# Kernel tuning notes

Measured on AMD Instinct MI355X. Metric: run time of the kernel, lower is better.

The kernel has to match this reference:

```python
import jax, jax.numpy as jnp
import numpy as np

S = 24; N = S * S; D = 1024; B = 4; H = 8; HD = D // H; K = 8
LN_EPS = 1e-5


def _spiral_indices(s, clockwise):
    inds = []
    top, bottom, left, right = 0, s - 1, 0, s - 1
    if clockwise:
        while top <= bottom and left <= right:
            for j in range(left, right + 1):
                inds.append((top, j))
            top += 1
            for i in range(top, bottom + 1):
                inds.append((i, right))
            right -= 1
            if top <= bottom:
                for j in range(right, left - 1, -1):
                    inds.append((bottom, j))
                bottom -= 1
            if left <= right:
                for i in range(bottom, top - 1, -1):
                    inds.append((i, left))
                left += 1
    else:
        while top <= bottom and left <= right:
            for i in range(top, bottom + 1):
                inds.append((i, left))
            left += 1
            for j in range(left, right + 1):
                inds.append((bottom, j))
            bottom -= 1
            if left <= right:
                for i in range(bottom, top - 1, -1):
                    inds.append((i, right))
                right -= 1
            if top <= bottom:
                for j in range(right, left - 1, -1):
                    inds.append((top, j))
                top += 1
    return np.array([i * s + j for i, j in inds], dtype=np.int32)


def _diag_indices(s, anti):
    idx = []
    for offset in (range(2 * s - 1) if anti else range(-(s - 1), s)):
        for i in range(s):
            j = (offset - i) if anti else (i + offset)
            if 0 <= j < s:
                idx.append(i * s + j)
    return np.array(idx, dtype=np.int32)


def _build_scan_indices(s):
    # Composite (scan + restore) permutation per direction: out_i = Linear_i(x[:, idx_i])
    ar = np.arange(s * s, dtype=np.int32).reshape(s, s)
    lr = ar.reshape(-1)                      # left_right: identity
    rl_scan = ar[:, ::-1].reshape(-1)        # right_left scan
    rl_restore = ar[:, ::-1].reshape(-1)     # restore flips width back
    rl = rl_scan[rl_restore]                 # composes to identity
    tb = ar.T.reshape(-1)                    # top_bottom (restore is plain view -> no inverse!)
    bt_scan = ar[::-1, :].T.reshape(-1)      # bottom_top scan: flip(transpose) flatten
    bt_restore = ar[::-1, :].reshape(-1)     # restore: view->transpose->flip(2)->transpose
    bt = bt_scan[bt_restore]
    dm = _diag_indices(s, anti=False)        # restore is plain view
    da = _diag_indices(s, anti=True)
    sc = _spiral_indices(s, clockwise=True)
    scc = _spiral_indices(s, clockwise=False)
    return np.stack([lr, rl, tb, bt, dm, da, sc, scc], axis=0)  # [8, N]


def setup_inputs() -> dict:
    key = jax.random.key(0)
    ks = jax.random.split(key, 12)
    sc = D ** -0.5
    return {
        "vision_features": jax.random.normal(ks[0], (B, N, D), dtype=jnp.float32),
        "dir_W": jax.random.normal(ks[1], (K, D, D), dtype=jnp.float32) * sc,
        "dir_b": jax.random.normal(ks[2], (K, D), dtype=jnp.float32) * 0.01,
        "in_proj_w": jax.random.normal(ks[3], (3 * D, D), dtype=jnp.float32) * sc,
        "in_proj_b": jax.random.normal(ks[4], (3 * D,), dtype=jnp.float32) * 0.01,
        "out_proj_w": jax.random.normal(ks[5], (D, D), dtype=jnp.float32) * sc,
        "out_proj_b": jax.random.normal(ks[6], (D,), dtype=jnp.float32) * 0.01,
        "fin_w": jax.random.normal(ks[7], (D, D), dtype=jnp.float32) * sc,
        "fin_b": jax.random.normal(ks[8], (D,), dtype=jnp.float32) * 0.01,
        "ln_g": jnp.ones((D,), dtype=jnp.float32),
        "ln_b": jnp.zeros((D,), dtype=jnp.float32),
        "scan_idx": jnp.asarray(_build_scan_indices(S)),  # [8, N] int32
    }


def reference(vision_features, dir_W, dir_b, in_proj_w, in_proj_b,
              out_proj_w, out_proj_b, fin_w, fin_b, ln_g, ln_b, scan_idx):
    b, n, d = vision_features.shape
    # Fused per-direction gather + batched GEMM: [B,8,N,D]
    gathered = vision_features[:, scan_idx]                     # [B,K,N,D]
    dirs = jnp.einsum('bknd,kde->bkne', gathered, dir_W) + dir_b[None, :, None, :]
    kv = dirs.reshape(b, K * n, d)                              # [B,8N,D]
    # MultiheadAttention (batch_first, 8 heads, eval -> no dropout)
    wq, wk, wv = in_proj_w[:d], in_proj_w[d:2 * d], in_proj_w[2 * d:]
    bq, bk, bv = in_proj_b[:d], in_proj_b[d:2 * d], in_proj_b[2 * d:]
    q = (vision_features @ wq.T + bq).reshape(b, n, H, HD).transpose(0, 2, 1, 3)
    k = (kv @ wk.T + bk).reshape(b, K * n, H, HD).transpose(0, 2, 1, 3)
    v = (kv @ wv.T + bv).reshape(b, K * n, H, HD).transpose(0, 2, 1, 3)
    scores = jnp.einsum('bhnd,bhmd->bhnm', q, k) / jnp.sqrt(jnp.asarray(HD, q.dtype))
    attn = jax.nn.softmax(scores, axis=-1)
    o = jnp.einsum('bhnm,bhmd->bhnd', attn, v).transpose(0, 2, 1, 3).reshape(b, n, d)
    fused = o @ out_proj_w.T + out_proj_b
    # output_projection: Linear -> LayerNorm (dropout inactive)
    y = fused @ fin_w.T + fin_b
    mu = jnp.mean(y, axis=-1, keepdims=True)
    var = jnp.mean(jnp.square(y - mu), axis=-1, keepdims=True)
    y = (y - mu) * jax.lax.rsqrt(var + LN_EPS) * ln_g + ln_b
    return y + vision_features
```

## Files before the change

kernel.cpp:

```cpp
#include <hip/hip_runtime.h>
#include <hip/hip_bf16.h>

typedef __attribute__((ext_vector_type(8))) short short8;
typedef __attribute__((ext_vector_type(4))) float f32x4;
typedef __attribute__((ext_vector_type(4))) int i32x4;

#define NTOK 576
#define DIM  1024
#define NB   4
#define NH   8
#define HD   128
#define KDIR 8
#define KN   4608
#define NSPLIT 8

__device__ __forceinline__ float us2f(unsigned short u) {
    unsigned int x = ((unsigned int)u) << 16;
    return __uint_as_float(x);
}
__device__ __forceinline__ unsigned short f2us(float f) {
    unsigned int x = __float_as_uint(f);
    unsigned int r = x + 0x7fffu + ((x >> 16) & 1u);
    return (unsigned short)(r >> 16);
}
__device__ __forceinline__ unsigned short cvt_bf16(float f) {
    unsigned int pk;
    asm("v_cvt_pk_bf16_f32 %0, %1, %2" : "=v"(pk) : "v"(f), "v"(f));
    return (unsigned short)(pk & 0xffffu);
}

typedef __attribute__((address_space(3))) unsigned int lds_uint;
typedef const __attribute__((address_space(1))) unsigned int glb_uint;
__device__ __forceinline__ void async16(const unsigned short* g, unsigned short* l) {
    __builtin_amdgcn_global_load_lds((glb_uint*)g, (lds_uint*)l, 16, 0, 0);
}
__device__ __forceinline__ void wait_vm0_barrier() {
    asm volatile("s_waitcnt vmcnt(0)" ::: "memory");
    __builtin_amdgcn_s_barrier();
    __builtin_amdgcn_sched_barrier(0);
}

__global__ void detect_kernel(const unsigned int* __restrict__ src, int* meta)
{
    if (threadIdx.x == 0) {
        int cnt = 0;
        for (int i = 0; i < 256; ++i) {
            unsigned u = src[(long)i * 16384] & 0xFFFFu;
            unsigned e = (u >> 7) & 0xFFu;
            cnt += (e >= 90 && e <= 150) ? 1 : 0;
        }
        meta[0] = (cnt >= 192) ? 1 : 0;
    }
}

struct ConvJobs {
    const void* src[10];
    unsigned short* dst[10];
    int n4[10];
    int bstart[10];
};
__global__ __launch_bounds__(256)
void conv_all(ConvJobs J, const int* __restrict__ meta)
{
    const int b = blockIdx.x;
    int ji = 0;
    #pragma unroll
    for (int i = 1; i < 10; ++i) if (b >= J.bstart[i]) ji = i;
    const long base = (long)(b - J.bstart[ji]) * 1024 + threadIdx.x;
    const long n4 = J.n4[ji];
    if (meta[0]) {
        const ushort4* s = (const ushort4*)J.src[ji];
        ushort4* d = (ushort4*)J.dst[ji];
        #pragma unroll
        for (int t = 0; t < 4; ++t) {
            long i = base + t * 256;
            if (i < n4) d[i] = s[i];
        }
    } else {
        const float4* s = (const float4*)J.src[ji];
        ushort4* d = (ushort4*)J.dst[ji];
        #pragma unroll
        for (int t = 0; t < 4; ++t) {
            long i = base + t * 256;
            if (i < n4) {
                float4 v = s[i];
                ushort4 o;
                o.x = f2us(v.x); o.y = f2us(v.y); o.z = f2us(v.z); o.w = f2us(v.w);
                d[i] = o;
            }
        }
    }
}

__global__ __launch_bounds__(256)
void transpose_conv(const void* __restrict__ src, unsigned short* __restrict__ dst,
                    const int* __restrict__ meta)
{
    const int k = blockIdx.y;
    const int ty = blockIdx.x >> 5, tx = blockIdx.x & 31;
    const int d0 = ty * 32, e0 = tx * 32;
    __shared__ float tl[32][33];
    const int t = threadIdx.x;
    const int row = t >> 3, c4 = (t & 7) * 4;
    const long sbase = ((long)k * 1024 + d0 + row) * 1024 + e0 + c4;
    if (meta[0]) {
        const unsigned short* s = (const unsigned short*)src;
        ushort4 v = *(const ushort4*)(s + sbase);
        tl[row][c4+0] = us2f(v.x); tl[row][c4+1] = us2f(v.y);
        tl[row][c4+2] = us2f(v.z); tl[row][c4+3] = us2f(v.w);
    } else {
        const float* s = (const float*)src;
        float4 v = *(const float4*)(s + sbase);
        tl[row][c4+0] = v.x; tl[row][c4+1] = v.y;
        tl[row][c4+2] = v.z; tl[row][c4+3] = v.w;
    }
    __syncthreads();
    ushort4 o;
    o.x = f2us(tl[c4+0][row]); o.y = f2us(tl[c4+1][row]);
    o.z = f2us(tl[c4+2][row]); o.w = f2us(tl[c4+3][row]);
    *(ushort4*)(dst + ((long)k * 1024 + e0 + row) * 1024 + d0 + c4) = o;
}

template<int MODE, int TN, int BM, int BN>
__global__ __launch_bounds__(256)
void gemm_glds(const unsigned short* __restrict__ A, const unsigned short* __restrict__ Bw,
               const unsigned short* __restrict__ bias, unsigned short* __restrict__ C,
               const unsigned short* __restrict__ B2, const unsigned short* __restrict__ bias2,
               unsigned short* __restrict__ C2,
               int M, long bStride, long biasStride)
{
    constexpr int MI = BM / 32, NI = BN / 32;
    const int z = blockIdx.y;
    const unsigned short* Bb;
    const unsigned short* Gb;
    if constexpr (MODE == 6) {
        Bb = (z < 8) ? Bw + (long)z * bStride : B2;
        Gb = (z < 8) ? bias + (long)z * biasStride : bias2;
    } else {
        Bb = Bw + (long)z * bStride;
        Gb = bias + (long)z * biasStride;
    }
    const int tm = blockIdx.x / TN;
    const int tn = blockIdx.x % TN;

    __shared__ __align__(16) unsigned short As[2][BM * 64];
    __shared__ __align__(16) unsigned short Bs[2][BN * 64];

    const int tid = threadIdx.x, lane = tid & 63, wid = tid >> 6;
    const int wm = wid >> 1, wn = wid & 1;
    const int r0 = lane & 15, hi = lane >> 4;
    const int lr = lane >> 3;
    const int lg = lane & 7;

    f32x4 zz = {0.f, 0.f, 0.f, 0.f};
    f32x4 acc[MI][NI];
    #pragma unroll
    for (int i = 0; i < MI; ++i)
        #pragma unroll
        for (int j = 0; j < NI; ++j) acc[i][j] = zz;

    const int sgc = ((lg ^ (lr & 7)) << 3);

    auto stage = [&](int k0, int buf) {
        #pragma unroll
        for (int j = 0; j < BM / 32; ++j) {
            int rb = wid * (BM / 4) + j * 8;
            async16(A + (long)(tm * BM + rb + lr) * 1024 + k0 + sgc, &As[buf][rb * 64]);
        }
        #pragma unroll
        for (int j = 0; j < BN / 32; ++j) {
            int rb = wid * (BN / 4) + j * 8;
            async16(Bb + (long)(tn * BN + rb + lr) * 1024 + k0 + sgc, &Bs[buf][rb * 64]);
        }
    };

    stage(0, 0);
    for (int kt = 0; kt < 16; ++kt) {
        wait_vm0_barrier();
        if (kt < 15) stage((kt + 1) * 64, (kt + 1) & 1);
        const unsigned short* Asb = As[kt & 1];
        const unsigned short* Bsb = Bs[kt & 1];
        __builtin_amdgcn_s_setprio(1);
        #pragma unroll
        for (int kd = 0; kd < 2; ++kd) {
            const int pg = ((kd * 4 + hi) ^ (r0 & 7)) << 3;
            short8 af[MI], bfr[NI];
            #pragma unroll
            for (int mi = 0; mi < MI; ++mi)
                af[mi] = *reinterpret_cast<const short8*>(&Asb[(wm * (BM/2) + mi * 16 + r0) * 64 + pg]);
            #pragma unroll
            for (int ni = 0; ni < NI; ++ni)
                bfr[ni] = *reinterpret_cast<const short8*>(&Bsb[(wn * (BN/2) + ni * 16 + r0) * 64 + pg]);
            #pragma unroll
            for (int mi = 0; mi < MI; ++mi)
                #pragma unroll
                for (int ni = 0; ni < NI; ++ni)
                    acc[mi][ni] = __builtin_amdgcn_mfma_f32_16x16x32_bf16(af[mi], bfr[ni], acc[mi][ni], 0, 0, 0);
        }
        __builtin_amdgcn_s_setprio(0);
    }

    const int jr = hi * 4;
    #pragma unroll
    for (int ni = 0; ni < NI; ++ni) {
        int cg = tn * BN + wn * (BN/2) + ni * 16 + r0;
        float bv = us2f(Gb[cg]);
        if constexpr (MODE == 5) {
            if (cg >= 1024) {
                int cg2 = cg - 1024;
                int h = cg2 >> 7, d = cg2 & 127;
                #pragma unroll
                for (int mi = 0; mi < MI; ++mi) {
                    int rgb = tm * BM + wm * (BM/2) + mi * 16 + jr;
                    int b = rgb / 4608, kv = rgb - b * 4608;
                    ushort4 o;
                    o.x = f2us(acc[mi][ni][0] + bv);
                    o.y = f2us(acc[mi][ni][1] + bv);
                    o.z = f2us(acc[mi][ni][2] + bv);
                    o.w = f2us(acc[mi][ni][3] + bv);
                    *(ushort4*)&C2[((long)(b * 8 + h) * 128 + d) * 4608 + kv] = o;
                }
                continue;
            }
        }
        #pragma unroll
        for (int mi = 0; mi < MI; ++mi) {
            #pragma unroll
            for (int j = 0; j < 4; ++j) {
                int rg = tm * BM + wm * (BM/2) + mi * 16 + jr + j;
                float val = acc[mi][ni][j] + bv;
                if constexpr (MODE == 0) {
                    C[(long)rg * 1024 + cg] = f2us(val);
                } else if constexpr (MODE == 5) {
                    int b = rg / 4608, kv = rg - b * 4608;
                    int h = cg >> 7, d = cg & 127;
                    C[((long)(b * 8 + h) * 4608 + kv) * 128 + d] = f2us(val);
                } else {
                    int b = rg / 576, n = rg - b * 576;
                    if (z == 8) {
                        int h = cg >> 7, d = cg & 127;
                        C2[((long)(b * 8 + h) * 576 + n) * 128 + d] = f2us(val);
                    } else {
                        C[((long)b * 4608 + (long)z * 576 + n) * 1024 + cg] = f2us(val);
                    }
                }
            }
        }
    }
}

__global__ __launch_bounds__(256)
void attn_kernel5(const unsigned short* __restrict__ Qh, const unsigned short* __restrict__ Kh,
                  const unsigned short* __restrict__ VTh, unsigned short* __restrict__ Opart,
                  float2* __restrict__ Ml)
{
    const int bid = blockIdx.x;
    const int logical = (bid & 7) * 288 + (bid >> 3);
    const int bhsp = logical / 9;
    const int qt = logical - bhsp * 9;
    const int bh = bhsp >> 3;
    const int sp = bhsp & 7;

    const int tid = threadIdx.x;
    const int lane = tid & 63, wid = tid >> 6;
    const int r0 = lane & 15, hi = lane >> 4;
    const int k8 = hi * 8;

    __shared__ __align__(16) unsigned short Ks[2][64 * 128];
    __shared__ __align__(16) unsigned short VT[2][128 * 64];

    const float SCL2 = 0.08838834764831845f * 1.4426950408889634f;
    short8 qf[4];
    {
        const long qoff = ((long)bh * NTOK + qt * 64 + wid * 16 + r0) * HD;
        #pragma unroll
        for (int kd = 0; kd < 4; ++kd) {
            short8 q = *reinterpret_cast<const short8*>(Qh + qoff + kd * 32 + k8);
            short8 qs;
            #pragma unroll
            for (int e = 0; e < 8; ++e)
                qs[e] = (short)cvt_bf16(us2f((unsigned short)q[e]) * SCL2);
            qf[kd] = qs;
        }
    }

    f32x4 zz = {0.f, 0.f, 0.f, 0.f};
    f32x4 oacc[8];
    #pragma unroll
    for (int i = 0; i < 8; ++i) oacc[i] = zz;
    float mrun = -1e30f, lrun = 0.f;

    const unsigned short* kbase0 = Kh + (long)bh * KN * HD;
    const unsigned short* vbase  = VTh + (long)bh * HD * KN;

    auto stage = [&](int kt, int buf) {
        const int kv0 = sp * (KN / NSPLIT) + kt * 64;
        const unsigned short* kb = kbase0 + (long)kv0 * HD;
        #pragma unroll
        for (int j = 0; j < 4; ++j) {
            int li = wid * 4 + j;
            int r = li * 4 + hi;
            int scK = (((lane & 15) ^ (r & 7)) << 3);
            async16(kb + (long)r * HD + scK, &Ks[buf][(li * 4) * 128]);
            int rv = li * 8 + (lane >> 3);
            int scV = (((lane & 7) ^ (rv & 7)) << 3);
            async16(vbase + (long)rv * KN + kv0 + scV, &VT[buf][(li * 8) * 64]);
        }
    };

    const int src0 = (lane & 15) + ((lane & 16) ? 32 : 0);
    const int src1 = src0 + 16;
    const bool selhi = lane >= 32;

    stage(0, 0);
    for (int kt = 0; kt < KN / NSPLIT / 64; ++kt) {
        wait_vm0_barrier();
        if (kt < KN / NSPLIT / 64 - 1) stage(kt + 1, (kt + 1) & 1);
        const unsigned short* Ksb = Ks[kt & 1];
        const unsigned short* VTb = VT[kt & 1];

        f32x4 s[4];
        #pragma unroll
        for (int nb = 0; nb < 4; ++nb) s[nb] = zz;
        __builtin_amdgcn_s_setprio(1);
        #pragma unroll
        for (int nb = 0; nb < 4; ++nb) {
            const int krow = nb * 16 + r0;
            #pragma unroll
            for (int kd = 0; kd < 4; ++kd) {
                short8 kf = *reinterpret_cast<const short8*>(
                    &Ksb[krow * 128 + (((kd * 4 + hi) ^ (r0 & 7)) << 3)]);
                s[nb] = __builtin_amdgcn_mfma_f32_16x16x32_bf16(kf, qf[kd], s[nb], 0, 0, 0);
            }
        }
        __builtin_amdgcn_s_setprio(0);

        float m0 = fmaxf(fmaxf(s[0][0], s[0][1]), fmaxf(s[0][2], s[0][3]));
        float m1 = fmaxf(fmaxf(s[1][0], s[1][1]), fmaxf(s[1][2], s[1][3]));
        float m2 = fmaxf(fmaxf(s[2][0], s[2][1]), fmaxf(s[2][2], s[2][3]));
        float m3 = fmaxf(fmaxf(s[3][0], s[3][1]), fmaxf(s[3][2], s[3][3]));
        float mt = fmaxf(fmaxf(m0, m1), fmaxf(m2, m3));
        mt = fmaxf(mt, __shfl_xor(mt, 16));
        mt = fmaxf(mt, __shfl_xor(mt, 32));
        if (!__all(mt - mrun <= 8.0f)) {
            float mn = fmaxf(mrun, mt);
            float scl = exp2f(mrun - mn);
            mrun = mn;
            lrun *= scl;
            #pragma unroll
            for (int db = 0; db < 8; ++db)
                #pragma unroll
                for (int j = 0; j < 4; ++j)
                    oacc[db][j] *= scl;
        }
        float p[4][4];
        float rt = 0.f;
        #pragma unroll
        for (int nb = 0; nb < 4; ++nb)
            #pragma unroll
            for (int j = 0; j < 4; ++j) {
                p[nb][j] = exp2f(s[nb][j] - mrun);
                rt += p[nb][j];
            }
        rt += __shfl_xor(rt, 16);
        rt += __shfl_xor(rt, 32);
        lrun += rt;

        unsigned pk0[4], pk1[4];
        #pragma unroll
        for (int nb = 0; nb < 4; ++nb) {
            asm("v_cvt_pk_bf16_f32 %0, %1, %2" : "=v"(pk0[nb]) : "v"(p[nb][0]), "v"(p[nb][1]));
            asm("v_cvt_pk_bf16_f32 %0, %1, %2" : "=v"(pk1[nb]) : "v"(p[nb][2]), "v"(p[nb][3]));
        }
        i32x4 pfrag[2];
        #pragma unroll
        for (int kd = 0; kd < 2; ++kd) {
            int a0 = __shfl((int)pk0[2*kd], src0), b0 = __shfl((int)pk0[2*kd+1], src0);
            int a1 = __shfl((int)pk1[2*kd], src0), b1 = __shfl((int)pk1[2*kd+1], src0);
            int a2 = __shfl((int)pk0[2*kd], src1), b2 = __shfl((int)pk0[2*kd+1], src1);
            int a3 = __shfl((int)pk1[2*kd], src1), b3 = __shfl((int)pk1[2*kd+1], src1);
            pfrag[kd][0] = selhi ? b0 : a0;
            pfrag[kd][1] = selhi ? b1 : a1;
            pfrag[kd][2] = selhi ? b2 : a2;
            pfrag[kd][3] = selhi ? b3 : a3;
        }

        __builtin_amdgcn_s_setprio(1);
        #pragma unroll
        for (int kd = 0; kd < 2; ++kd) {
            short8 pf = *reinterpret_cast<const short8*>(&pfrag[kd]);
            const int pg = ((kd * 4 + hi) ^ (r0 & 7)) << 3;
            #pragma unroll
            for (int db = 0; db < 8; ++db) {
                short8 vf = *reinterpret_cast<const short8*>(&VTb[(db * 16 + r0) * 64 + pg]);
                oacc[db] = __builtin_amdgcn_mfma_f32_16x16x32_bf16(vf, pf, oacc[db], 0, 0, 0);
            }
        }
        __builtin_amdgcn_s_setprio(0);
    }

    const float inv = 1.f / lrun;
    const long po = ((long)(sp * 32 + bh) * NTOK + qt * 64 + wid * 16 + r0) * HD;
    #pragma unroll
    for (int db = 0; db < 8; ++db) {
        ushort4 o;
        o.x = f2us(oacc[db][0] * inv);
        o.y = f2us(oacc[db][1] * inv);
        o.z = f2us(oacc[db][2] * inv);
        o.w = f2us(oacc[db][3] * inv);
        *(ushort4*)&Opart[po + db * 16 + hi * 4] = o;
    }
    if (lane < 16) {
        const long mo = (long)(sp * 32 + bh) * NTOK + qt * 64 + wid * 16 + r0;
        Ml[mo] = make_float2(mrun, lrun);
    }
}

__global__ __launch_bounds__(256)
void attn_reduce(const unsigned short* __restrict__ Opart, const float2* __restrict__ Ml,
                 unsigned short* __restrict__ Ob)
{
    const int qt = blockIdx.x, bh = blockIdx.y;
    const int t = threadIdx.x;
    const int rl = t >> 2, dc = (t & 3) * 32;
    const int q = qt * 64 + rl;

    float m[NSPLIT], l[NSPLIT];
    float M = -1e30f;
    #pragma unroll
    for (int sp = 0; sp < NSPLIT; ++sp) {
        float2 v = Ml[(long)(sp * 32 + bh) * NTOK + q];
        m[sp] = v.x; l[sp] = v.y;
        M = fmaxf(M, v.x);
    }
    float w[NSPLIT], denom = 0.f;
    #pragma unroll
    for (int sp = 0; sp < NSPLIT; ++sp) {
        w[sp] = l[sp] * exp2f(m[sp] - M);
        denom += w[sp];
    }
    const float inv = 1.f / denom;
    const int b = bh >> 3, h = bh & 7;
    #pragma unroll
    for (int dj = 0; dj < 4; ++dj) {
        float a[8];
        #pragma unroll
        for (int e = 0; e < 8; ++e) a[e] = 0.f;
        #pragma unroll
        for (int sp = 0; sp < NSPLIT; ++sp) {
            short8 v = *reinterpret_cast<const short8*>(
                &Opart[((long)(sp * 32 + bh) * NTOK + q) * HD + dc + dj * 8]);
            #pragma unroll
            for (int e = 0; e < 8; ++e)
                a[e] += w[sp] * us2f((unsigned short)v[e]);
        }
        short8 o;
        #pragma unroll
        for (int e = 0; e < 8; ++e) o[e] = (short)f2us(a[e] * inv);
        *reinterpret_cast<short8*>(&Ob[((long)b * NTOK + q) * 1024 + h * 128 + dc + dj * 8]) = o;
    }
}

__global__ __launch_bounds__(256)
void ln2_kernel(const unsigned short* __restrict__ Y, const unsigned short* __restrict__ g,
                const unsigned short* __restrict__ be, const unsigned short* __restrict__ vis,
                void* __restrict__ dout, const int* __restrict__ meta)
{
    const int row = blockIdx.x;
    const int tid = threadIdx.x;
    const int lane = tid & 63, wid = tid >> 6;
    const unsigned short* yr = Y + (long)row * DIM;
    ushort4 raw = reinterpret_cast<const ushort4*>(yr)[tid];
    float v[4];
    v[0] = us2f(raw.x); v[1] = us2f(raw.y); v[2] = us2f(raw.z); v[3] = us2f(raw.w);
    float s1 = 0.f, s2 = 0.f;
    #pragma unroll
    for (int i = 0; i < 4; ++i) { s1 += v[i]; s2 += v[i] * v[i]; }
    #pragma unroll
    for (int off = 1; off < 64; off <<= 1) {
        s1 += __shfl_xor(s1, off);
        s2 += __shfl_xor(s2, off);
    }
    __shared__ float red[2][4];
    if (lane == 0) { red[0][wid] = s1; red[1][wid] = s2; }
    __syncthreads();
    s1 = red[0][0] + red[0][1] + red[0][2] + red[0][3];
    s2 = red[1][0] + red[1][1] + red[1][2] + red[1][3];
    const float mu = s1 * (1.f / DIM);
    const float var = s2 * (1.f / DIM) - mu * mu;
    const float inv = rsqrtf(var + 1e-5f);
    ushort4 gg = reinterpret_cast<const ushort4*>(g)[tid];
    ushort4 bb = reinterpret_cast<const ushort4*>(be)[tid];
    ushort4 vv = reinterpret_cast<const ushort4*>(vis + (long)row * DIM)[tid];
    float o0 = (v[0] - mu) * inv * us2f(gg.x) + us2f(bb.x) + us2f(vv.x);
    float o1 = (v[1] - mu) * inv * us2f(gg.y) + us2f(bb.y) + us2f(vv.y);
    float o2 = (v[2] - mu) * inv * us2f(gg.z) + us2f(bb.z) + us2f(vv.z);
    float o3 = (v[3] - mu) * inv * us2f(gg.w) + us2f(bb.w) + us2f(vv.w);
    if (meta[0]) {
        ushort4 o;
        o.x = f2us(o0); o.y = f2us(o1); o.z = f2us(o2); o.w = f2us(o3);
        reinterpret_cast<ushort4*>((unsigned short*)dout + (long)row * DIM)[tid] = o;
    } else {
        float4 o = make_float4(o0, o1, o2, o3);
        reinterpret_cast<float4*>((float*)dout + (long)row * DIM)[tid] = o;
    }
}

extern "C" void kernel_launch(void* const* d_in, const int* in_sizes, int n_in,
                              void* d_out, int out_size, void* d_ws, size_t ws_size,
                              hipStream_t stream)
{
    unsigned long long w = (unsigned long long)d_ws;
    int* meta = (int*)w; w += 256;

    const int cidx[10] = {0, 2, 3, 4, 5, 6, 7, 8, 9, 10};
    const long csz[10] = {
        (long)NB * NTOK * DIM,
        (long)KDIR * DIM,
        3L * DIM * DIM,
        3L * DIM,
        (long)DIM * DIM,
        DIM,
        (long)DIM * DIM,
        DIM, DIM, DIM
    };
    unsigned short* cv[10];
    for (int i = 0; i < 10; ++i) {
        cv[i] = (unsigned short*)w;
        w += (csz[i] * 2 + 255) & ~255ULL;
    }
    unsigned short* dWT = (unsigned short*)w; w += (long)KDIR * DIM * DIM * 2;

    const size_t big = (size_t)NB * KDIR * NTOK * DIM * 2;
    const size_t sml = (size_t)NB * NTOK * DIM * 2;
    unsigned short* dirs = (unsigned short*)w; w += big;
    unsigned short* Kh   = (unsigned short*)w; w += big;
    unsigned short* VTh  = (unsigned short*)w; w += big;
    unsigned short* Qh   = (unsigned short*)w; w += sml;
    unsigned short* Ob   = (unsigned short*)w; w += sml;
    unsigned short* Fu   = (unsigned short*)w; w += sml;
    unsigned short* Y2   = (unsigned short*)w; w += sml;
    float2* Ml = (float2*)w; w += (long)NSPLIT * 32 * NTOK * sizeof(float2);
    unsigned short* Opart = dirs;

    const unsigned short* vision = cv[0];
    const unsigned short* dirb = cv[1];
    const unsigned short* inW = cv[2];
    const unsigned short* inB = cv[3];
    const unsigned short* outW = cv[4];
    const unsigned short* outB = cv[5];
    const unsigned short* finW = cv[6];
    const unsigned short* finB = cv[7];
    const unsigned short* lng = cv[8];
    const unsigned short* lnbt = cv[9];

    dim3 blk(256, 1, 1);

    detect_kernel<<<dim3(1), dim3(64), 0, stream>>>((const unsigned int*)d_in[1], meta);

    ConvJobs J;
    int bacc = 0;
    for (int i = 0; i < 10; ++i) {
        J.src[i] = d_in[cidx[i]];
        J.dst[i] = cv[i];
        J.n4[i] = (int)(csz[i] / 4);
        J.bstart[i] = bacc;
        bacc += (int)((csz[i] / 4 + 1023) / 1024);
    }
    conv_all<<<dim3(bacc), blk, 0, stream>>>(J, meta);
    transpose_conv<<<dim3(1024, KDIR), blk, 0, stream>>>(d_in[1], dWT, meta);

    gemm_glds<6, 8, 128, 128><<<dim3(18 * 8, 9), blk, 0, stream>>>(
        vision, dWT, dirb, dirs, inW, inB, Qh, NB * NTOK, (long)DIM * DIM, DIM);

    gemm_glds<5, 16, 128, 128><<<dim3(144 * 16, 1), blk, 0, stream>>>(
        dirs, inW + DIM * DIM, inB + DIM, Kh, nullptr, nullptr, VTh, NB * KN, 0L, 0L);

    attn_kernel5<<<dim3(9 * 32 * NSPLIT), blk, 0, stream>>>(Qh, Kh, VTh, Opart, Ml);

    attn_reduce<<<dim3(9, 32), blk, 0, stream>>>(Opart, Ml, Ob);

    gemm_glds<0, 16, 64, 64><<<dim3(36 * 16, 1), blk, 0, stream>>>(
        Ob, outW, outB, Fu, nullptr, nullptr, nullptr, NB * NTOK, 0L, 0L);

    gemm_glds<0, 16, 64, 64><<<dim3(36 * 16, 1), blk, 0, stream>>>(
        Fu, finW, finB, Y2, nullptr, nullptr, nullptr, NB * NTOK, 0L, 0L);

    ln2_kernel<<<dim3(NB * NTOK), blk, 0, stream>>>(Y2, lng, lnbt, vision, d_out, meta);
}
```

Before: 391.2 us.

## Rework attention kernel: halve KV split, fold Q scale into GEMM, drop P shuffles

Moves the softmax scale multiply on Q into the QKV projection epilogue, so the attention kernel loads Q fragments directly. The KV split count drops from 8 to 4, which doubles the tiles per block and halves the partial outputs the reduce kernel must combine. The cross-lane P fragment shuffle is replaced by reading V^T in a permuted k-order that matches the MFMA accumulator layout. Row-sum reductions are deferred to the end, and the row-max shuffles happen only on the rescale path. Staging addresses are precomputed as pointer increments. Fewer blocks may lower occupancy and load balance, and attn_reduce must be correct for the new NSPLIT.

```diff
diff --git a/kernel.cpp b/kernel.cpp
--- a/kernel.cpp
+++ b/kernel.cpp
@@ -2,6 +2,7 @@
 #include <hip/hip_bf16.h>
 
 typedef __attribute__((ext_vector_type(8))) short short8;
+typedef __attribute__((ext_vector_type(4))) short short4v;
 typedef __attribute__((ext_vector_type(4))) float f32x4;
 typedef __attribute__((ext_vector_type(4))) int i32x4;
 
@@ -12,7 +13,8 @@
 #define HD   128
 #define KDIR 8
 #define KN   4608
-#define NSPLIT 8
+#define NSPLIT 4
+#define NT 18
 
 __device__ __forceinline__ float us2f(unsigned short u) {
     unsigned int x = ((unsigned int)u) << 16;
@@ -22,11 +24,6 @@
     unsigned int x = __float_as_uint(f);
     unsigned int r = x + 0x7fffu + ((x >> 16) & 1u);
     return (unsigned short)(r >> 16);
-}
-__device__ __forceinline__ unsigned short cvt_bf16(float f) {
-    unsigned int pk;
-    asm("v_cvt_pk_bf16_f32 %0, %1, %2" : "=v"(pk) : "v"(f), "v"(f));
-    return (unsigned short)(pk & 0xffffu);
 }
 
 typedef __attribute__((address_space(3))) unsigned int lds_uint;
@@ -200,6 +197,7 @@
         __builtin_amdgcn_s_setprio(0);
     }
 
+    const float QSCL = 0.08838834764831845f * 1.4426950408889634f;
     const int jr = hi * 4;
     #pragma unroll
     for (int ni = 0; ni < NI; ++ni) {
@@ -239,7 +237,7 @@
                     int b = rg / 576, n = rg - b * 576;
                     if (z == 8) {
                         int h = cg >> 7, d = cg & 127;
-                        C2[((long)(b * 8 + h) * 576 + n) * 128 + d] = f2us(val);
+                        C2[((long)(b * 8 + h) * 576 + n) * 128 + d] = f2us(val * QSCL);
                     } else {
                         C[((long)b * 4608 + (long)z * 576 + n) * 1024 + cg] = f2us(val);
                     }
@@ -250,16 +248,16 @@
 }
 
 __global__ __launch_bounds__(256)
-void attn_kernel5(const unsigned short* __restrict__ Qh, const unsigned short* __restrict__ Kh,
+void attn_kernel6(const unsigned short* __restrict__ Qh, const unsigned short* __restrict__ Kh,
                   const unsigned short* __restrict__ VTh, unsigned short* __restrict__ Opart,
                   float2* __restrict__ Ml)
 {
     const int bid = blockIdx.x;
-    const int logical = (bid & 7) * 288 + (bid >> 3);
+    const int logical = (bid & 7) * 144 + (bid >> 3);
     const int bhsp = logical / 9;
     const int qt = logical - bhsp * 9;
-    const int bh = bhsp >> 3;
-    const int sp = bhsp & 7;
+    const int bh = bhsp >> 2;
+    const int sp = bhsp & 3;
 
     const int tid = threadIdx.x;
     const int lane = tid & 63, wid = tid >> 6;
@@ -269,19 +267,12 @@
     __shared__ __align__(16) unsigned short Ks[2][64 * 128];
     __shared__ __align__(16) unsigned short VT[2][128 * 64];
 
-    const float SCL2 = 0.08838834764831845f * 1.4426950408889634f;
     short8 qf[4];
     {
         const long qoff = ((long)bh * NTOK + qt * 64 + wid * 16 + r0) * HD;
         #pragma unroll
-        for (int kd = 0; kd < 4; ++kd) {
-            short8 q = *reinterpret_cast<const short8*>(Qh + qoff + kd * 32 + k8);
-            short8 qs;
-            #pragma unroll
-            for (int e = 0; e < 8; ++e)
-                qs[e] = (short)cvt_bf16(us2f((unsigned short)q[e]) * SCL2);
-            qf[kd] = qs;
-        }
+        for (int kd = 0; kd < 4; ++kd)
+            qf[kd] = *reinterpret_cast<const short8*>(Qh + qoff + kd * 32 + k8);
     }
 
     f32x4 zz = {0.f, 0.f, 0.f, 0.f};
@@ -290,32 +281,27 @@
     for (int i = 0; i < 8; ++i) oacc[i] = zz;
     float mrun = -1e30f, lrun = 0.f;
 
-    const unsigned short* kbase0 = Kh + (long)bh * KN * HD;
-    const unsigned short* vbase  = VTh + (long)bh * HD * KN;
-
-    auto stage = [&](int kt, int buf) {
-        const int kv0 = sp * (KN / NSPLIT) + kt * 64;
-        const unsigned short* kb = kbase0 + (long)kv0 * HD;
+    int offK[4], offV[4];
+    #pragma unroll
+    for (int j = 0; j < 4; ++j) {
+        offK[j] = (wid * 16 + 4 * j + hi) * 128 + (((lane & 15) ^ ((4 * j + hi) & 7)) << 3);
+        offV[j] = (wid * 32 + 8 * j + (lane >> 3)) * KN + (((lane & 7) ^ (lane >> 3)) << 3);
+    }
+    const unsigned short* kp = Kh + (long)bh * KN * HD + (long)(sp * (KN / NSPLIT)) * HD;
+    const unsigned short* vp = VTh + (long)bh * HD * KN + sp * (KN / NSPLIT);
+
+    auto stage = [&](int buf) {
         #pragma unroll
         for (int j = 0; j < 4; ++j) {
-            int li = wid * 4 + j;
-            int r = li * 4 + hi;
-            int scK = (((lane & 15) ^ (r & 7)) << 3);
-            async16(kb + (long)r * HD + scK, &Ks[buf][(li * 4) * 128]);
-            int rv = li * 8 + (lane >> 3);
-            int scV = (((lane & 7) ^ (rv & 7)) << 3);
-            async16(vbase + (long)rv * KN + kv0 + scV, &VT[buf][(li * 8) * 64]);
+            async16(kp + offK[j], &Ks[buf][(wid * 16 + 4 * j) * 128]);
+            async16(vp + offV[j], &VT[buf][(wid * 32 + 8 * j) * 64]);
         }
     };
 
-    const int src0 = (lane & 15) + ((lane & 16) ? 32 : 0);
-    const int src1 = src0 + 16;
-    const bool selhi = lane >= 32;
-
-    stage(0, 0);
-    for (int kt = 0; kt < KN / NSPLIT / 64; ++kt) {
+    stage(0);
+    for (int kt = 0; kt < NT; ++kt) {
         wait_vm0_barrier();
-        if (kt < KN / NSPLIT / 64 - 1) stage(kt + 1, (kt + 1) & 1);
+        if (kt < NT - 1) { kp += 64 * HD; vp += 64; stage((kt + 1) & 1); }
         const unsigned short* Ksb = Ks[kt & 1];
         const unsigned short* VTb = VT[kt & 1];
 
@@ -335,15 +321,14 @@
         }
         __builtin_amdgcn_s_setprio(0);
 
-        float m0 = fmaxf(fmaxf(s[0][0], s[0][1]), fmaxf(s[0][2], s[0][3]));
-        float m1 = fmaxf(fmaxf(s[1][0], s[1][1]), fmaxf(s[1][2], s[1][3]));
-        float m2 = fmaxf(fmaxf(s[2][0], s[2][1]), fmaxf(s[2][2], s[2][3]));
-        float m3 = fmaxf(fmaxf(s[3][0], s[3][1]), fmaxf(s[3][2], s[3][3]));
-        float mt = fmaxf(fmaxf(m0, m1), fmaxf(m2, m3));
-        mt = fmaxf(mt, __shfl_xor(mt, 16));
-        mt = fmaxf(mt, __shfl_xor(mt, 32));
+        float mt = fmaxf(fmaxf(fmaxf(s[0][0], s[0][1]), fmaxf(s[0][2], s[0][3])),
+                   fmaxf(fmaxf(fmaxf(s[1][0], s[1][1]), fmaxf(s[1][2], s[1][3])),
+                   fmaxf(fmaxf(fmaxf(s[2][0], s[2][1]), fmaxf(s[2][2], s[2][3])),
+                         fmaxf(fmaxf(s[3][0], s[3][1]), fmaxf(s[3][2], s[3][3])))));
         if (!__all(mt - mrun <= 8.0f)) {
-            float mn = fmaxf(mrun, mt);
+            float mr = fmaxf(mt, __shfl_xor(mt, 16));
+            mr = fmaxf(mr, __shfl_xor(mr, 32));
+            float mn = fmaxf(mrun, mr);
             float scl = exp2f(mrun - mn);
             mrun = mn;
             lrun *= scl;
@@ -362,8 +347,6 @@
                 p[nb][j] = exp2f(s[nb][j] - mrun);
                 rt += p[nb][j];
             }
-        rt += __shfl_xor(rt, 16);
-        rt += __shfl_xor(rt, 32);
         lrun += rt;
 
         unsigned pk0[4], pk1[4];
@@ -372,33 +355,32 @@
             asm("v_cvt_pk_bf16_f32 %0, %1, %2" : "=v"(pk0[nb]) : "v"(p[nb][0]), "v"(p[nb][1]));
             asm("v_cvt_pk_bf16_f32 %0, %1, %2" : "=v"(pk1[nb]) : "v"(p[nb][2]), "v"(p[nb][3]));
         }
-        i32x4 pfrag[2];
+
+        __builtin_amdgcn_s_setprio(1);
         #pragma unroll
         for (int kd = 0; kd < 2; ++kd) {
-            int a0 = __shfl((int)pk0[2*kd], src0), b0 = __shfl((int)pk0[2*kd+1], src0);
-            int a1 = __shfl((int)pk1[2*kd], src0), b1 = __shfl((int)pk1[2*kd+1], src0);
-            int a2 = __shfl((int)pk0[2*kd], src1), b2 = __shfl((int)pk0[2*kd+1], src1);
-            int a3 = __shfl((int)pk1[2*kd], src1), b3 = __shfl((int)pk1[2*kd+1], src1);
-            pfrag[kd][0] = selhi ? b0 : a0;
-            pfrag[kd][1] = selhi ? b1 : a1;
-            pfrag[kd][2] = selhi ? b2 : a2;
-            pfrag[kd][3] = selhi ? b3 : a3;
-        }
-
-        __builtin_amdgcn_s_setprio(1);
-        #pragma unroll
-        for (int kd = 0; kd < 2; ++kd) {
-            short8 pf = *reinterpret_cast<const short8*>(&pfrag[kd]);
-            const int pg = ((kd * 4 + hi) ^ (r0 & 7)) << 3;
+            i32x4 fr;
+            fr[0] = (int)pk0[2 * kd];
+            fr[1] = (int)pk1[2 * kd];
+            fr[2] = (int)pk0[2 * kd + 1];
+            fr[3] = (int)pk1[2 * kd + 1];
+            short8 pf = *reinterpret_cast<short8*>(&fr);
+            const int cg0 = (hi >> 1) + 4 * kd;
+            const int sub = (hi & 1) << 2;
             #pragma unroll
             for (int db = 0; db < 8; ++db) {
-                short8 vf = *reinterpret_cast<const short8*>(&VTb[(db * 16 + r0) * 64 + pg]);
+                const int vrow = (db * 16 + r0) * 64;
+                short4v lo = *(const short4v*)&VTb[vrow + ((cg0 ^ (r0 & 7)) << 3) + sub];
+                short4v hh = *(const short4v*)&VTb[vrow + (((cg0 + 2) ^ (r0 & 7)) << 3) + sub];
+                short8 vf = {lo[0], lo[1], lo[2], lo[3], hh[0], hh[1], hh[2], hh[3]};
                 oacc[db] = __builtin_amdgcn_mfma_f32_16x16x32_bf16(vf, pf, oacc[db], 0, 0, 0);
             }
         }
         __builtin_amdgcn_s_setprio(0);
     }
 
+    lrun += __shfl_xor(lrun, 16);
+    lrun += __shfl_xor(lrun, 32);
     const float inv = 1.f / lrun;
     const long po = ((long)(sp * 32 + bh) * NTOK + qt * 64 + wid * 16 + r0) * HD;
     #pragma unroll
@@ -576,7 +558,7 @@
     gemm_glds<5, 16, 128, 128><<<dim3(144 * 16, 1), blk, 0, stream>>>(
         dirs, inW + DIM * DIM, inB + DIM, Kh, nullptr, nullptr, VTh, NB * KN, 0L, 0L);
 
-    attn_kernel5<<<dim3(9 * 32 * NSPLIT), blk, 0, stream>>>(Qh, Kh, VTh, Opart, Ml);
+    attn_kernel6<<<dim3(9 * 32 * NSPLIT), blk, 0, stream>>>(Qh, Kh, VTh, Opart, Ml);
 
     attn_reduce<<<dim3(9, 32), blk, 0, stream>>>(Opart, Ml, Ob);
 
```

New measurement: 389.7 us. Within noise of the previous version (-0.4%).
